# Kernel tuning notes

Measured on AMD Instinct MI355X. Metric: run time of the kernel, lower is better.

The kernel has to match this reference:

```python
import jax, jax.numpy as jnp
import numpy as np

N_NODES = 100000
N_EDGES = 800000
B = 4000            # number of pair subgraphs
GNN_IN = 428        # embed_dim(300) + 128 structural features
H = 64              # GIN hidden_channels
HID = 512           # PATH_DIM
EMB = 300           # numberbatch embedding dim
NUM_CLS = 151       # VG object classes
N_LAYERS = 3


def setup_inputs() -> dict:
    key = jax.random.key(0)
    ks = jax.random.split(key, 32)
    inp = {
        "pred_pairs": jax.random.randint(ks[0], (B, 2), 0, NUM_CLS, dtype=jnp.int32),
        "x": jax.random.normal(ks[1], (N_NODES, GNN_IN), dtype=jnp.float32),
        "edge_index": jax.random.randint(ks[2], (2, N_EDGES), 0, N_NODES, dtype=jnp.int32),
        "batch_ids": jnp.sort(jax.random.randint(ks[3], (N_NODES,), 0, B, dtype=jnp.int32)),
        "entity_embed": jax.random.normal(ks[4], (NUM_CLS, EMB), dtype=jnp.float32) * 0.05,
    }
    dins = [GNN_IN, H, H]
    for l in range(N_LAYERS):
        inp[f"w1_{l}"] = jax.random.normal(ks[5 + 4 * l], (dins[l], H), dtype=jnp.float32) * 0.05
        inp[f"b1_{l}"] = jnp.zeros((H,), dtype=jnp.float32)
        inp[f"w2_{l}"] = jax.random.normal(ks[6 + 4 * l], (H, H), dtype=jnp.float32) * 0.05
        inp[f"b2_{l}"] = jnp.zeros((H,), dtype=jnp.float32)
    inp["lin_w"] = jax.random.normal(ks[20], (H, HID), dtype=jnp.float32) * 0.05
    inp["lin_b"] = jnp.zeros((HID,), dtype=jnp.float32)
    inp["final_w"] = jax.random.normal(ks[21], (2 * EMB + HID, HID), dtype=jnp.float32) * 0.05
    inp["final_b"] = jnp.zeros((HID,), dtype=jnp.float32)
    return inp


def _gin_conv(h, src, dst, w1, b1, w2, b2):
    # GIN (eps=0): h_i' = MLP(h_i + sum_{j->i} h_j)
    agg = jax.ops.segment_sum(h[src], dst, num_segments=N_NODES)  # [N, d]
    z = h + agg
    z = jax.nn.relu(z @ w1 + b1)
    return jax.nn.relu(z @ w2 + b2)


def reference(pred_pairs, x, edge_index, batch_ids, entity_embed,
              w1_0, b1_0, w2_0, b2_0,
              w1_1, b1_1, w2_1, b2_1,
              w1_2, b1_2, w2_2, b2_2,
              lin_w, lin_b, final_w, final_b):
    src, dst = edge_index[0], edge_index[1]
    h = x
    for (w1, b1, w2, b2) in ((w1_0, b1_0, w2_0, b2_0),
                             (w1_1, b1_1, w2_1, b2_1),
                             (w1_2, b1_2, w2_2, b2_2)):
        h = _gin_conv(h, src, dst, w1, b1, w2, b2)
    # graph-level mean pooling over batch segments
    pooled = jax.ops.segment_sum(h, batch_ids, num_segments=B)              # [B, H]
    counts = jax.ops.segment_sum(jnp.ones((N_NODES,), h.dtype), batch_ids,
                                 num_segments=B)                            # [B]
    pooled = pooled / jnp.maximum(counts, 1.0)[:, None]
    emb = pooled @ lin_w + lin_b                                            # [B, HID]
    original = entity_embed[pred_pairs].reshape(B, 2 * EMB)                 # [B, 600]
    out = jnp.concatenate([emb, original], axis=1) @ final_w + final_b      # [B, HID]
    return out
```

## Files before the change

### kernel.cpp

```cpp
#include <hip/hip_runtime.h>
#include <hip/hip_bf16.h>

#define N_NODES 100000
#define N_EDGES 800000
#define BGRAPH  4000
#define GNN_IN  428
#define HDIM    64
#define HID     512
#define EMBD    300
#define AIN     1112
#define CAP     48
#define LSTR    72

typedef unsigned short u16;
typedef short bf16x8 __attribute__((ext_vector_type(8)));
typedef float f32x4  __attribute__((ext_vector_type(4)));

__device__ __forceinline__ u16 f2bf(float f) {
    union { float f; unsigned int u; } v; v.f = f;
    unsigned int r = v.u + 0x7FFFu + ((v.u >> 16) & 1u);
    return (u16)(r >> 16);
}
__device__ __forceinline__ float bf2f(u16 u) {
    union { unsigned int u; float f; } v; v.u = ((unsigned int)u) << 16;
    return v.f;
}

__global__ void k_prep_w0(const float* __restrict__ w, u16* __restrict__ w0T) {
    const int idx = blockIdx.x * 256 + threadIdx.x;
    if (idx >= 64 * 448) return;
    const int n = idx / 448, k = idx - n * 448;
    w0T[idx] = (k < GNN_IN) ? f2bf(w[k * 64 + n]) : (u16)0;
}
__global__ void k_prep_fw(const float* __restrict__ fw, u16* __restrict__ fwT) {
    const int idx = blockIdx.x * 256 + threadIdx.x;
    if (idx >= 512 * 1120) return;
    const int n = idx / 1120, k = idx - n * 1120;
    fwT[idx] = (k < AIN) ? f2bf(fw[(size_t)k * 512 + n]) : (u16)0;
}
__global__ void k_prep_w64(const float* __restrict__ w, u16* __restrict__ wT) {
    const int idx = blockIdx.x * 256 + threadIdx.x;
    const int k = idx >> 6, o = idx & 63;
    wT[o * 64 + k] = f2bf(w[idx]);
}

__global__ __launch_bounds__(256) void k_gemm_xw(const float* __restrict__ x,
                                                 const u16* __restrict__ w0T,
                                                 u16* __restrict__ y) {
    const int t = threadIdx.x;
    const int lane = t & 63, wave = t >> 6;
    const int q = lane >> 4, m = lane & 15;
    const int n0 = blockIdx.x * 64;
    const int row = min(n0 + wave * 16 + m, N_NODES - 1);
    const float* __restrict__ xr = &x[(size_t)row * GNN_IN];

    f32x4 acc[4];
#pragma unroll
    for (int c = 0; c < 4; ++c) acc[c] = (f32x4){0.f, 0.f, 0.f, 0.f};

    for (int k0 = 0; k0 < 448; k0 += 32) {
        const int ka = k0 + q * 8;
        float4 va = {0.f, 0.f, 0.f, 0.f}, vb = {0.f, 0.f, 0.f, 0.f};
        if (ka + 4 <= GNN_IN) va = *reinterpret_cast<const float4*>(xr + ka);
        if (ka + 8 <= GNN_IN) vb = *reinterpret_cast<const float4*>(xr + ka + 4);
        bf16x8 a;
        a[0] = (short)f2bf(va.x); a[1] = (short)f2bf(va.y);
        a[2] = (short)f2bf(va.z); a[3] = (short)f2bf(va.w);
        a[4] = (short)f2bf(vb.x); a[5] = (short)f2bf(vb.y);
        a[6] = (short)f2bf(vb.z); a[7] = (short)f2bf(vb.w);
#pragma unroll
        for (int c = 0; c < 4; ++c) {
            const bf16x8 b = *reinterpret_cast<const bf16x8*>(&w0T[(c * 16 + m) * 448 + ka]);
            acc[c] = __builtin_amdgcn_mfma_f32_16x16x32_bf16(a, b, acc[c], 0, 0, 0);
        }
    }
#pragma unroll
    for (int c = 0; c < 4; ++c)
#pragma unroll
        for (int r = 0; r < 4; ++r) {
            const int rr = n0 + wave * 16 + q * 4 + r;
            if (rr < N_NODES) y[(size_t)rr * 64 + c * 16 + m] = f2bf(acc[c][r]);
        }
}

__global__ void k_fill(const int* __restrict__ ei, int* __restrict__ deg,
                       int* __restrict__ csr2) {
    const int e = blockIdx.x * blockDim.x + threadIdx.x;
    if (e >= N_EDGES) return;
    const int s = ei[e];
    const int d = ei[N_EDGES + e];
    const int slot = atomicAdd(&deg[d], 1);
    if (slot < CAP) csr2[d * CAP + slot] = s;
}

__global__ void k_counts(const int* __restrict__ bids, float* __restrict__ counts) {
    const int n = blockIdx.x * blockDim.x + threadIdx.x;
    if (n >= N_NODES) return;
    atomicAdd(&counts[bids[n]], 1.0f);
}

__device__ __forceinline__ float gather16p(const u16* __restrict__ hin,
                                           const int* __restrict__ lst,
                                           int dg, int lane, float u) {
    const int4* l4 = reinterpret_cast<const int4*>(lst);
    const int4 ia = l4[0], ib = l4[1], ic = l4[2], id4 = l4[3];
    int id[16] = {ia.x, ia.y, ia.z, ia.w, ib.x, ib.y, ib.z, ib.w,
                  ic.x, ic.y, ic.z, ic.w, id4.x, id4.y, id4.z, id4.w};
    float v[16];
#pragma unroll
    for (int i = 0; i < 16; ++i) {
        const bool ok = (i < dg);
        const int idx = ok ? id[i] : 0;
        v[i] = bf2f(hin[(size_t)idx * 64 + lane]) * (ok ? 1.f : 0.f);
    }
#pragma unroll
    for (int i = 0; i < 16; ++i) u += v[i];
    if (__builtin_expect(dg > 16, 0)) {
        for (int e = 16; e < dg; e += 8) {
            const int4 a = l4[e >> 2];
            const int4 b = l4[(e >> 2) + 1];
            int id2[8] = {a.x, a.y, a.z, a.w, b.x, b.y, b.z, b.w};
#pragma unroll
            for (int i = 0; i < 8; ++i) {
                const bool ok = (e + i < dg);
                const int idx = ok ? id2[i] : 0;
                u += bf2f(hin[(size_t)idx * 64 + lane]) * (ok ? 1.f : 0.f);
            }
        }
    }
    return u;
}

__global__ __launch_bounds__(256, 4) void k_gin0(const u16* __restrict__ y,
                                                 const int* __restrict__ deg,
                                                 const int* __restrict__ csr2,
                                                 const float* __restrict__ b1,
                                                 const u16* __restrict__ w2T,
                                                 const float* __restrict__ b2,
                                                 u16* __restrict__ hout) {
    __shared__ u16 zs[64 * LSTR];
    const int t = threadIdx.x;
    const int lane = t & 63, wave = t >> 6;
    const int q = lane >> 4, m = lane & 15;
    const int n0 = blockIdx.x * 64;
    const int base = n0 + wave * 16;
    const float b1v = b1[lane];
#pragma unroll 2
    for (int j = 0; j < 16; ++j) {
        const int n = min(base + j, N_NODES - 1);
        const int dg = min(deg[n], CAP);
        float u = bf2f(y[(size_t)n * 64 + lane]);
        u = gather16p(y, &csr2[n * CAP], dg, lane, u);
        zs[(wave * 16 + j) * LSTR + lane] = f2bf(fmaxf(u + b1v, 0.f));
    }
    f32x4 acc[4];
#pragma unroll
    for (int c = 0; c < 4; ++c) acc[c] = (f32x4){0.f, 0.f, 0.f, 0.f};
    const bf16x8 a0 = *reinterpret_cast<const bf16x8*>(&zs[(wave * 16 + m) * LSTR + q * 8]);
    const bf16x8 a1 = *reinterpret_cast<const bf16x8*>(&zs[(wave * 16 + m) * LSTR + 32 + q * 8]);
#pragma unroll
    for (int c = 0; c < 4; ++c) {
        const bf16x8 bb0 = *reinterpret_cast<const bf16x8*>(&w2T[(c * 16 + m) * 64 + q * 8]);
        const bf16x8 bb1 = *reinterpret_cast<const bf16x8*>(&w2T[(c * 16 + m) * 64 + 32 + q * 8]);
        acc[c] = __builtin_amdgcn_mfma_f32_16x16x32_bf16(a0, bb0, acc[c], 0, 0, 0);
        acc[c] = __builtin_amdgcn_mfma_f32_16x16x32_bf16(a1, bb1, acc[c], 0, 0, 0);
    }
#pragma unroll
    for (int c = 0; c < 4; ++c) {
        const float bb = b2[c * 16 + m];
#pragma unroll
        for (int r = 0; r < 4; ++r) {
            const int n = n0 + wave * 16 + q * 4 + r;
            if (n < N_NODES) hout[(size_t)n * 64 + c * 16 + m] = f2bf(fmaxf(acc[c][r] + bb, 0.f));
        }
    }
}

__device__ __forceinline__ void gin_mfma2(const u16* __restrict__ hin,
                                          const int* __restrict__ deg,
                                          const int* __restrict__ csr2,
                                          const u16* __restrict__ w1T,
                                          const float* __restrict__ b1,
                                          const u16* __restrict__ w2T,
                                          u16* us, u16* zs,
                                          int n0, int t, f32x4 acc[4]) {
    const int lane = t & 63, wave = t >> 6;
    const int q = lane >> 4, m = lane & 15;
    const int base = n0 + wave * 16;
#pragma unroll 2
    for (int j = 0; j < 16; ++j) {
        const int n = min(base + j, N_NODES - 1);
        const int dg = min(deg[n], CAP);
        float u = bf2f(hin[(size_t)n * 64 + lane]);
        u = gather16p(hin, &csr2[n * CAP], dg, lane, u);
        us[(wave * 16 + j) * LSTR + lane] = f2bf(u);
    }
    f32x4 z[4];
#pragma unroll
    for (int c = 0; c < 4; ++c) z[c] = (f32x4){0.f, 0.f, 0.f, 0.f};
    {
        const bf16x8 a0 = *reinterpret_cast<const bf16x8*>(&us[(wave * 16 + m) * LSTR + q * 8]);
        const bf16x8 a1 = *reinterpret_cast<const bf16x8*>(&us[(wave * 16 + m) * LSTR + 32 + q * 8]);
#pragma unroll
        for (int c = 0; c < 4; ++c) {
            const bf16x8 bb0 = *reinterpret_cast<const bf16x8*>(&w1T[(c * 16 + m) * 64 + q * 8]);
            const bf16x8 bb1 = *reinterpret_cast<const bf16x8*>(&w1T[(c * 16 + m) * 64 + 32 + q * 8]);
            z[c] = __builtin_amdgcn_mfma_f32_16x16x32_bf16(a0, bb0, z[c], 0, 0, 0);
            z[c] = __builtin_amdgcn_mfma_f32_16x16x32_bf16(a1, bb1, z[c], 0, 0, 0);
        }
    }
#pragma unroll
    for (int c = 0; c < 4; ++c) {
        const float bb = b1[c * 16 + m];
#pragma unroll
        for (int r = 0; r < 4; ++r)
            zs[(wave * 16 + q * 4 + r) * LSTR + c * 16 + m] = f2bf(fmaxf(z[c][r] + bb, 0.f));
    }
#pragma unroll
    for (int c = 0; c < 4; ++c) acc[c] = (f32x4){0.f, 0.f, 0.f, 0.f};
    {
        const bf16x8 a0 = *reinterpret_cast<const bf16x8*>(&zs[(wave * 16 + m) * LSTR + q * 8]);
        const bf16x8 a1 = *reinterpret_cast<const bf16x8*>(&zs[(wave * 16 + m) * LSTR + 32 + q * 8]);
#pragma unroll
        for (int c = 0; c < 4; ++c) {
            const bf16x8 bb0 = *reinterpret_cast<const bf16x8*>(&w2T[(c * 16 + m) * 64 + q * 8]);
            const bf16x8 bb1 = *reinterpret_cast<const bf16x8*>(&w2T[(c * 16 + m) * 64 + 32 + q * 8]);
            acc[c] = __builtin_amdgcn_mfma_f32_16x16x32_bf16(a0, bb0, acc[c], 0, 0, 0);
            acc[c] = __builtin_amdgcn_mfma_f32_16x16x32_bf16(a1, bb1, acc[c], 0, 0, 0);
        }
    }
}

__global__ __launch_bounds__(256, 4) void k_gin(const u16* __restrict__ hin,
                                                const int* __restrict__ deg,
                                                const int* __restrict__ csr2,
                                                const u16* __restrict__ w1T,
                                                const float* __restrict__ b1,
                                                const u16* __restrict__ w2T,
                                                const float* __restrict__ b2,
                                                u16* __restrict__ hout) {
    __shared__ u16 us[64 * LSTR];
    __shared__ u16 zs[64 * LSTR];
    const int t = threadIdx.x;
    const int lane = t & 63, wave = t >> 6;
    const int q = lane >> 4, m = lane & 15;
    const int n0 = blockIdx.x * 64;
    f32x4 acc[4];
    gin_mfma2(hin, deg, csr2, w1T, b1, w2T, us, zs, n0, t, acc);
#pragma unroll
    for (int c = 0; c < 4; ++c) {
        const float bb = b2[c * 16 + m];
#pragma unroll
        for (int r = 0; r < 4; ++r) {
            const int n = n0 + wave * 16 + q * 4 + r;
            if (n < N_NODES) hout[(size_t)n * 64 + c * 16 + m] = f2bf(fmaxf(acc[c][r] + bb, 0.f));
        }
    }
}

__global__ __launch_bounds__(256, 4) void k_gin_pool(const u16* __restrict__ hin,
                                                     const int* __restrict__ deg,
                                                     const int* __restrict__ csr2,
                                                     const u16* __restrict__ w1T,
                                                     const float* __restrict__ b1,
                                                     const u16* __restrict__ w2T,
                                                     const float* __restrict__ b2,
                                                     const int* __restrict__ bids,
                                                     float* __restrict__ pooled) {
    __shared__ u16 us[64 * LSTR];
    __shared__ u16 zs[64 * LSTR];
    const int t = threadIdx.x;
    const int lane = t & 63, wave = t >> 6;
    const int q = lane >> 4, m = lane & 15;
    const int n0 = blockIdx.x * 64;
    f32x4 acc[4];
    gin_mfma2(hin, deg, csr2, w1T, b1, w2T, us, zs, n0, t, acc);
#pragma unroll
    for (int c = 0; c < 4; ++c) {
        const float bb = b2[c * 16 + m];
#pragma unroll
        for (int r = 0; r < 4; ++r)
            us[(wave * 16 + q * 4 + r) * LSTR + c * 16 + m] = f2bf(fmaxf(acc[c][r] + bb, 0.f));
    }
    const int base = n0 + wave * 16;
    if (base < N_NODES) {
        float s = 0.f;
        int cur = bids[base];
        for (int j = 0; j < 16; ++j) {
            const int n = base + j;
            if (n >= N_NODES) break;
            const int b = bids[n];
            const float h = bf2f(us[(wave * 16 + j) * LSTR + lane]);
            if (b != cur) {
                atomicAdd(&pooled[cur * 64 + lane], s);
                cur = b; s = h;
            } else {
                s += h;
            }
        }
        atomicAdd(&pooled[cur * 64 + lane], s);
    }
}

__global__ __launch_bounds__(256) void k_emb(const float* __restrict__ pooled,
                                             const float* __restrict__ counts,
                                             const float* __restrict__ lw,
                                             const float* __restrict__ lb,
                                             u16* __restrict__ A) {
    __shared__ float prow[8][64];
    const int b0 = blockIdx.x * 8;
    const int t = threadIdx.x;
    const int lane = t & 63, wave = t >> 6;
    for (int i = 0; i < 2; ++i) {
        const int r = i * 4 + wave;
        const int b = b0 + r;
        const float c = fmaxf(counts[b], 1.0f);
        prow[r][lane] = pooled[b * 64 + lane] / c;
    }
    __syncthreads();
    for (int o = t; o < 512; o += 256) {
        float acc[8];
#pragma unroll
        for (int r = 0; r < 8; ++r) acc[r] = lb[o];
        for (int k = 0; k < 64; ++k) {
            const float wv = lw[k * 512 + o];
#pragma unroll
            for (int r = 0; r < 8; ++r) acc[r] += prow[r][k] * wv;
        }
#pragma unroll
        for (int r = 0; r < 8; ++r) A[(size_t)(b0 + r) * AIN + o] = f2bf(acc[r]);
    }
}

__global__ void k_orig(const int* __restrict__ pp, const float* __restrict__ ee,
                       u16* __restrict__ A) {
    const int idx = blockIdx.x * blockDim.x + threadIdx.x;
    if (idx >= BGRAPH * 600) return;
    const int b = idx / 600;
    const int j = idx - b * 600;
    const int which = (j >= 300) ? 1 : 0;
    const int cls = pp[b * 2 + which];
    A[(size_t)b * AIN + 512 + j] = f2bf(ee[cls * 300 + (j - which * 300)]);
}

__global__ __launch_bounds__(256) void k_final(const u16* __restrict__ A,
                                               const u16* __restrict__ fwT,
                                               const float* __restrict__ fb,
                                               float* __restrict__ out) {
    __shared__ u16 as[64 * 40];
    const int t = threadIdx.x;
    const int lane = t & 63, wave = t >> 6;
    const int q = lane >> 4, m = lane & 15;
    const int r0 = blockIdx.x * 64, c0 = blockIdx.y * 64;

    f32x4 acc[4];
#pragma unroll
    for (int c = 0; c < 4; ++c) acc[c] = (f32x4){0.f, 0.f, 0.f, 0.f};

    const int row = t >> 2, seg = t & 3;
    for (int k0 = 0; k0 < 1120; k0 += 32) {
        const int gr = r0 + row, gk = k0 + seg * 8;
        uint4 v = {0u, 0u, 0u, 0u};
        if (gr < BGRAPH && gk < AIN)
            v = *reinterpret_cast<const uint4*>(&A[(size_t)gr * AIN + gk]);
        *reinterpret_cast<uint4*>(&as[row * 40 + seg * 8]) = v;
        __syncthreads();
        const bf16x8 a = *reinterpret_cast<const bf16x8*>(&as[(wave * 16 + m) * 40 + q * 8]);
#pragma unroll
        for (int c = 0; c < 4; ++c) {
            const bf16x8 b = *reinterpret_cast<const bf16x8*>(&fwT[(size_t)(c0 + c * 16 + m) * 1120 + k0 + q * 8]);
            acc[c] = __builtin_amdgcn_mfma_f32_16x16x32_bf16(a, b, acc[c], 0, 0, 0);
        }
        __syncthreads();
    }
#pragma unroll
    for (int c = 0; c < 4; ++c) {
        const float bb = fb[c0 + c * 16 + m];
#pragma unroll
        for (int r = 0; r < 4; ++r) {
            const int rr = r0 + wave * 16 + q * 4 + r;
            if (rr < BGRAPH) out[(size_t)rr * 512 + c0 + c * 16 + m] = acc[c][r] + bb;
        }
    }
}

extern "C" void kernel_launch(void* const* d_in, const int* in_sizes, int n_in,
                              void* d_out, int out_size, void* d_ws, size_t ws_size,
                              hipStream_t stream) {
    const int*   pred_pairs = (const int*)d_in[0];
    const float* x          = (const float*)d_in[1];
    const int*   ei         = (const int*)d_in[2];
    const int*   bids       = (const int*)d_in[3];
    const float* ee         = (const float*)d_in[4];
    const float* w1_0 = (const float*)d_in[5];
    const float* b1_0 = (const float*)d_in[6];
    const float* w2_0 = (const float*)d_in[7];
    const float* b2_0 = (const float*)d_in[8];
    const float* w1_1 = (const float*)d_in[9];
    const float* b1_1 = (const float*)d_in[10];
    const float* w2_1 = (const float*)d_in[11];
    const float* b2_1 = (const float*)d_in[12];
    const float* w1_2 = (const float*)d_in[13];
    const float* b1_2 = (const float*)d_in[14];
    const float* w2_2 = (const float*)d_in[15];
    const float* b2_2 = (const float*)d_in[16];
    const float* lin_w   = (const float*)d_in[17];
    const float* lin_b   = (const float*)d_in[18];
    const float* final_w = (const float*)d_in[19];
    const float* final_b = (const float*)d_in[20];
    float* out = (float*)d_out;

    u16*   Y      = (u16*)d_ws;
    u16*   Hb     = Y + (size_t)N_NODES * 64;
    int*   csr2   = (int*)(Hb + (size_t)N_NODES * 64);
    int*   deg    = csr2 + (size_t)N_NODES * CAP;
    float* pooled = (float*)(deg + N_NODES);
    float* counts = pooled + (size_t)BGRAPH * 64;
    u16*   A      = (u16*)(counts + BGRAPH);
    u16*   w0T    = A + (size_t)BGRAPH * AIN;
    u16*   fwT    = w0T + 64 * 448;
    u16*   w2T0   = fwT + (size_t)512 * 1120;
    u16*   w1T1   = w2T0 + 4096;
    u16*   w2T1   = w1T1 + 4096;
    u16*   w1T2   = w2T1 + 4096;
    u16*   w2T2   = w1T2 + 4096;

    hipMemsetAsync(deg, 0, (size_t)(N_NODES + BGRAPH * 64 + BGRAPH) * sizeof(int), stream);

    k_prep_w0<<<(64 * 448 + 255) / 256, 256, 0, stream>>>(w1_0, w0T);
    k_prep_fw<<<(512 * 1120 + 255) / 256, 256, 0, stream>>>(final_w, fwT);
    k_prep_w64<<<16, 256, 0, stream>>>(w2_0, w2T0);
    k_prep_w64<<<16, 256, 0, stream>>>(w1_1, w1T1);
    k_prep_w64<<<16, 256, 0, stream>>>(w2_1, w2T1);
    k_prep_w64<<<16, 256, 0, stream>>>(w1_2, w1T2);
    k_prep_w64<<<16, 256, 0, stream>>>(w2_2, w2T2);
    k_fill<<<(N_EDGES + 255) / 256, 256, 0, stream>>>(ei, deg, csr2);
    k_counts<<<(N_NODES + 255) / 256, 256, 0, stream>>>(bids, counts);
    k_gemm_xw<<<(N_NODES + 63) / 64, 256, 0, stream>>>(x, w0T, Y);
    k_gin0<<<(N_NODES + 63) / 64, 256, 0, stream>>>(Y, deg, csr2, b1_0, w2T0, b2_0, Hb);
    k_gin<<<(N_NODES + 63) / 64, 256, 0, stream>>>(Hb, deg, csr2, w1T1, b1_1, w2T1, b2_1, Y);
    k_gin_pool<<<(N_NODES + 63) / 64, 256, 0, stream>>>(Y, deg, csr2, w1T2, b1_2, w2T2, b2_2, bids, pooled);
    k_emb<<<BGRAPH / 8, 256, 0, stream>>>(pooled, counts, lin_w, lin_b, A);
    k_orig<<<(BGRAPH * 600 + 255) / 256, 256, 0, stream>>>(pred_pairs, ee, A);
    k_final<<<dim3((BGRAPH + 63) / 64, 8), 256, 0, stream>>>(A, fwT, final_b, out);
}
```

Baseline: 604.8 us.

## Merge prep kernels into one launch and software-pipeline loads in xw GEMM

```diff
diff --git a/kernel.cpp b/kernel.cpp
--- a/kernel.cpp
+++ b/kernel.cpp
@@ -26,22 +26,63 @@
     return v.f;
 }
 
-__global__ void k_prep_w0(const float* __restrict__ w, u16* __restrict__ w0T) {
-    const int idx = blockIdx.x * 256 + threadIdx.x;
-    if (idx >= 64 * 448) return;
-    const int n = idx / 448, k = idx - n * 448;
-    w0T[idx] = (k < GNN_IN) ? f2bf(w[k * 64 + n]) : (u16)0;
-}
-__global__ void k_prep_fw(const float* __restrict__ fw, u16* __restrict__ fwT) {
-    const int idx = blockIdx.x * 256 + threadIdx.x;
-    if (idx >= 512 * 1120) return;
-    const int n = idx / 1120, k = idx - n * 1120;
-    fwT[idx] = (k < AIN) ? f2bf(fw[(size_t)k * 512 + n]) : (u16)0;
-}
-__global__ void k_prep_w64(const float* __restrict__ w, u16* __restrict__ wT) {
-    const int idx = blockIdx.x * 256 + threadIdx.x;
-    const int k = idx >> 6, o = idx & 63;
-    wT[o * 64 + k] = f2bf(w[idx]);
+#define R_W0T   (64 * 448)
+#define R_FWT   (512 * 1120)
+#define R_W64   (5 * 4096)
+#define R_ORIG  (BGRAPH * 600)
+#define PREP_TOT (R_W0T + R_FWT + R_W64 + R_ORIG)
+
+__global__ void k_prep_all(const float* __restrict__ w1_0, const float* __restrict__ final_w,
+                           const float* __restrict__ w2_0, const float* __restrict__ w1_1,
+                           const float* __restrict__ w2_1, const float* __restrict__ w1_2,
+                           const float* __restrict__ w2_2,
+                           const int* __restrict__ pp, const float* __restrict__ ee,
+                           u16* __restrict__ w0T, u16* __restrict__ fwT,
+                           u16* __restrict__ wT5, u16* __restrict__ A) {
+    int idx = blockIdx.x * 256 + threadIdx.x;
+    if (idx < R_W0T) {
+        const int n = idx / 448, k = idx - n * 448;
+        w0T[idx] = (k < GNN_IN) ? f2bf(w1_0[k * 64 + n]) : (u16)0;
+        return;
+    }
+    idx -= R_W0T;
+    if (idx < R_FWT) {
+        const int n = idx / 1120, k = idx - n * 1120;
+        fwT[idx] = (k < AIN) ? f2bf(final_w[(size_t)k * 512 + n]) : (u16)0;
+        return;
+    }
+    idx -= R_FWT;
+    if (idx < R_W64) {
+        const int which = idx >> 12;
+        const int r = idx & 4095;
+        const float* w = (which == 0) ? w2_0 : (which == 1) ? w1_1
+                       : (which == 2) ? w2_1 : (which == 3) ? w1_2 : w2_2;
+        wT5[(which << 12) + ((r & 63) << 6) + (r >> 6)] = f2bf(w[r]);
+        return;
+    }
+    idx -= R_W64;
+    if (idx < R_ORIG) {
+        const int b = idx / 600;
+        const int j = idx - b * 600;
+        const int which = (j >= 300) ? 1 : 0;
+        const int cls = pp[b * 2 + which];
+        A[(size_t)b * AIN + 512 + j] = f2bf(ee[cls * 300 + (j - which * 300)]);
+    }
+}
+
+__global__ void k_graph(const int* __restrict__ ei, int* __restrict__ deg,
+                        int* __restrict__ csr2,
+                        const int* __restrict__ bids, float* __restrict__ counts) {
+    const int e = blockIdx.x * blockDim.x + threadIdx.x;
+    if (e < N_EDGES) {
+        const int s = ei[e];
+        const int d = ei[N_EDGES + e];
+        const int slot = atomicAdd(&deg[d], 1);
+        if (slot < CAP) csr2[d * CAP + slot] = s;
+    }
+    if (e < N_NODES) {
+        atomicAdd(&counts[bids[e]], 1.0f);
+    }
 }
 
 __global__ __launch_bounds__(256) void k_gemm_xw(const float* __restrict__ x,
@@ -58,22 +99,41 @@
 #pragma unroll
     for (int c = 0; c < 4; ++c) acc[c] = (f32x4){0.f, 0.f, 0.f, 0.f};
 
-    for (int k0 = 0; k0 < 448; k0 += 32) {
-        const int ka = k0 + q * 8;
-        float4 va = {0.f, 0.f, 0.f, 0.f}, vb = {0.f, 0.f, 0.f, 0.f};
-        if (ka + 4 <= GNN_IN) va = *reinterpret_cast<const float4*>(xr + ka);
-        if (ka + 8 <= GNN_IN) vb = *reinterpret_cast<const float4*>(xr + ka + 4);
+    float4 xa[4][2];
+    bf16x8 wb[3][4];
+
+    auto ldx = [&](int tt, float4 dst[2]) {
+        const int ka = tt * 32 + q * 8;
+        float4 a = {0.f, 0.f, 0.f, 0.f}, b = {0.f, 0.f, 0.f, 0.f};
+        if (ka + 4 <= GNN_IN) a = *reinterpret_cast<const float4*>(xr + ka);
+        if (ka + 8 <= GNN_IN) b = *reinterpret_cast<const float4*>(xr + ka + 4);
+        dst[0] = a; dst[1] = b;
+    };
+    auto ldb = [&](int tt, bf16x8 dst[4]) {
+        const int ka = tt * 32 + q * 8;
+#pragma unroll
+        for (int c = 0; c < 4; ++c)
+            dst[c] = *reinterpret_cast<const bf16x8*>(&w0T[(c * 16 + m) * 448 + ka]);
+    };
+
+    ldx(0, xa[0]); ldx(1, xa[1]); ldx(2, xa[2]);
+    ldb(0, wb[0]); ldb(1, wb[1]);
+
+#pragma unroll
+    for (int tt = 0; tt < 14; ++tt) {
+        if (tt + 3 < 14) ldx(tt + 3, xa[(tt + 3) % 4]);
+        if (tt + 2 < 14) ldb(tt + 2, wb[(tt + 2) % 3]);
+        const float4 va = xa[tt % 4][0], vb = xa[tt % 4][1];
         bf16x8 a;
         a[0] = (short)f2bf(va.x); a[1] = (short)f2bf(va.y);
         a[2] = (short)f2bf(va.z); a[3] = (short)f2bf(va.w);
         a[4] = (short)f2bf(vb.x); a[5] = (short)f2bf(vb.y);
         a[6] = (short)f2bf(vb.z); a[7] = (short)f2bf(vb.w);
 #pragma unroll
-        for (int c = 0; c < 4; ++c) {
-            const bf16x8 b = *reinterpret_cast<const bf16x8*>(&w0T[(c * 16 + m) * 448 + ka]);
-            acc[c] = __builtin_amdgcn_mfma_f32_16x16x32_bf16(a, b, acc[c], 0, 0, 0);
-        }
-    }
+        for (int c = 0; c < 4; ++c)
+            acc[c] = __builtin_amdgcn_mfma_f32_16x16x32_bf16(a, wb[tt % 3][c], acc[c], 0, 0, 0);
+    }
+
 #pragma unroll
     for (int c = 0; c < 4; ++c)
 #pragma unroll
@@ -81,22 +141,6 @@
             const int rr = n0 + wave * 16 + q * 4 + r;
             if (rr < N_NODES) y[(size_t)rr * 64 + c * 16 + m] = f2bf(acc[c][r]);
         }
-}
-
-__global__ void k_fill(const int* __restrict__ ei, int* __restrict__ deg,
-                       int* __restrict__ csr2) {
-    const int e = blockIdx.x * blockDim.x + threadIdx.x;
-    if (e >= N_EDGES) return;
-    const int s = ei[e];
-    const int d = ei[N_EDGES + e];
-    const int slot = atomicAdd(&deg[d], 1);
-    if (slot < CAP) csr2[d * CAP + slot] = s;
-}
-
-__global__ void k_counts(const int* __restrict__ bids, float* __restrict__ counts) {
-    const int n = blockIdx.x * blockDim.x + threadIdx.x;
-    if (n >= N_NODES) return;
-    atomicAdd(&counts[bids[n]], 1.0f);
 }
 
 __device__ __forceinline__ float gather16p(const u16* __restrict__ hin,
@@ -330,17 +374,6 @@
 #pragma unroll
         for (int r = 0; r < 8; ++r) A[(size_t)(b0 + r) * AIN + o] = f2bf(acc[r]);
     }
-}
-
-__global__ void k_orig(const int* __restrict__ pp, const float* __restrict__ ee,
-                       u16* __restrict__ A) {
-    const int idx = blockIdx.x * blockDim.x + threadIdx.x;
-    if (idx >= BGRAPH * 600) return;
-    const int b = idx / 600;
-    const int j = idx - b * 600;
-    const int which = (j >= 300) ? 1 : 0;
-    const int cls = pp[b * 2 + which];
-    A[(size_t)b * AIN + 512 + j] = f2bf(ee[cls * 300 + (j - which * 300)]);
 }
 
 __global__ __launch_bounds__(256) void k_final(const u16* __restrict__ A,
@@ -419,7 +452,8 @@
     u16*   A      = (u16*)(counts + BGRAPH);
     u16*   w0T    = A + (size_t)BGRAPH * AIN;
     u16*   fwT    = w0T + 64 * 448;
-    u16*   w2T0   = fwT + (size_t)512 * 1120;
+    u16*   wT5    = fwT + (size_t)512 * 1120;
+    u16*   w2T0   = wT5;
     u16*   w1T1   = w2T0 + 4096;
     u16*   w2T1   = w1T1 + 4096;
     u16*   w1T2   = w2T1 + 4096;
@@ -427,20 +461,14 @@
 
     hipMemsetAsync(deg, 0, (size_t)(N_NODES + BGRAPH * 64 + BGRAPH) * sizeof(int), stream);
 
-    k_prep_w0<<<(64 * 448 + 255) / 256, 256, 0, stream>>>(w1_0, w0T);
-    k_prep_fw<<<(512 * 1120 + 255) / 256, 256, 0, stream>>>(final_w, fwT);
-    k_prep_w64<<<16, 256, 0, stream>>>(w2_0, w2T0);
-    k_prep_w64<<<16, 256, 0, stream>>>(w1_1, w1T1);
-    k_prep_w64<<<16, 256, 0, stream>>>(w2_1, w2T1);
-    k_prep_w64<<<16, 256, 0, stream>>>(w1_2, w1T2);
-    k_prep_w64<<<16, 256, 0, stream>>>(w2_2, w2T2);
-    k_fill<<<(N_EDGES + 255) / 256, 256, 0, stream>>>(ei, deg, csr2);
-    k_counts<<<(N_NODES + 255) / 256, 256, 0, stream>>>(bids, counts);
+    k_prep_all<<<(PREP_TOT + 255) / 256, 256, 0, stream>>>(
+        w1_0, final_w, w2_0, w1_1, w2_1, w1_2, w2_2, pred_pairs, ee,
+        w0T, fwT, wT5, A);
+    k_graph<<<(N_EDGES + 255) / 256, 256, 0, stream>>>(ei, deg, csr2, bids, counts);
     k_gemm_xw<<<(N_NODES + 63) / 64, 256, 0, stream>>>(x, w0T, Y);
     k_gin0<<<(N_NODES + 63) / 64, 256, 0, stream>>>(Y, deg, csr2, b1_0, w2T0, b2_0, Hb);
     k_gin<<<(N_NODES + 63) / 64, 256, 0, stream>>>(Hb, deg, csr2, w1T1, b1_1, w2T1, b2_1, Y);
     k_gin_pool<<<(N_NODES + 63) / 64, 256, 0, stream>>>(Y, deg, csr2, w1T2, b1_2, w2T2, b2_2, bids, pooled);
     k_emb<<<BGRAPH / 8, 256, 0, stream>>>(pooled, counts, lin_w, lin_b, A);
-    k_orig<<<(BGRAPH * 600 + 255) / 256, 256, 0, stream>>>(pred_pairs, ee, A);
     k_final<<<dim3((BGRAPH + 63) / 64, 8), 256, 0, stream>>>(A, fwT, final_b, out);
 }
```

Measured after the change: 597.0 us. Within noise of the previous version (-1.3%).
